# Kernel optimization log

Hardware: AMD Instinct MI355X
Metric: run time of the kernel (lower is better)

The kernel has to match this reference:

```python
import jax, jax.numpy as jnp
import numpy as np

N, E, D, H, A = 50000, 800000, 128, 256, 16


def setup_inputs() -> dict:
    key = jax.random.key(0)
    ks = jax.random.split(key, 16)
    s = 0.05
    return {
        "x": jax.random.normal(ks[0], (N, D), jnp.float32),
        "edge_index": jax.random.randint(ks[1], (2, E), 0, N, dtype=jnp.int32),
        "edge_attr": jax.random.normal(ks[2], (E, A), jnp.float32),
        # GCNConv 1 (input_dim -> hidden_dim): lin weight (no bias) + conv bias
        "W1": jax.random.normal(ks[3], (D, H), jnp.float32) * s,
        "b1": jnp.zeros((H,), jnp.float32),
        # GCNConv 2 (hidden_dim -> input_dim)
        "W2": jax.random.normal(ks[4], (H, D), jnp.float32) * s,
        "b2": jnp.zeros((D,), jnp.float32),
        # output_layer MLP: D -> H -> D
        "Wo1": jax.random.normal(ks[5], (D, H), jnp.float32) * s,
        "bo1": jnp.zeros((H,), jnp.float32),
        "Wo2": jax.random.normal(ks[6], (H, D), jnp.float32) * s,
        "bo2": jnp.zeros((D,), jnp.float32),
        # edge_predictor MLP: 2D+A -> H -> A
        "We1": jax.random.normal(ks[7], (2 * D + A, H), jnp.float32) * s,
        "be1": jnp.zeros((H,), jnp.float32),
        "We2": jax.random.normal(ks[8], (H, A), jnp.float32) * s,
        "be2": jnp.zeros((A,), jnp.float32),
    }


def reference(x, edge_index, edge_attr, W1, b1, W2, b2, Wo1, bo1, Wo2, bo2,
              We1, be1, We2, be2):
    n = x.shape[0]
    row, col = edge_index[0], edge_index[1]
    # GCNConv default: add self-loops, symmetric normalization deg^-1/2 A deg^-1/2
    loop = jnp.arange(n, dtype=row.dtype)
    row_f = jnp.concatenate([row, loop])
    col_f = jnp.concatenate([col, loop])
    deg = jax.ops.segment_sum(jnp.ones_like(col_f, dtype=x.dtype), col_f,
                              num_segments=n)
    dinv = jnp.where(deg > 0, jax.lax.rsqrt(jnp.maximum(deg, 1.0)), 0.0)
    norm = dinv[row_f] * dinv[col_f]  # [E+N]

    def gcn(h, W, b):
        h = h @ W                                # [n, out]
        msg = h[row_f] * norm[:, None]           # gather + scale
        agg = jax.ops.segment_sum(msg, col_f, num_segments=n)  # scatter-add
        return agg + b

    h = jax.nn.relu(gcn(x, W1, b1))
    h = jax.nn.relu(gcn(h, W2, b2))
    h = jax.nn.relu(h @ Wo1 + bo1) @ Wo2 + bo2   # output_layer MLP

    # edge predictor: gather endpoint features, concat with edge_attr, MLP
    edge_input = jnp.concatenate([h[row], h[col], edge_attr], axis=1)
    ea = jax.nn.relu(edge_input @ We1 + be1) @ We2 + be2
    return h, ea
```

## Files before the change

kernel.cpp:

```cpp
#include <hip/hip_runtime.h>
#include <hip/hip_bf16.h>

#define N_NODES 50000
#define N_EDGES 800000
#define DIM_D   128
#define DIM_H   256
#define DIM_A   16

typedef unsigned short u16;
typedef __attribute__((ext_vector_type(4))) float f4;
typedef __attribute__((ext_vector_type(8))) short s8;
typedef __attribute__((ext_vector_type(4))) short s4;

__device__ __forceinline__ u16 f2bf(float f) {
    union { float f; unsigned u; } v; v.f = f;
    unsigned r = v.u + 0x7FFFu + ((v.u >> 16) & 1u);
    return (u16)(r >> 16);
}
__device__ __forceinline__ float bf2f(u16 s) {
    union { unsigned u; float f; } v; v.u = ((unsigned)s) << 16; return v.f;
}
__device__ __forceinline__ s8 zero_s8() {
    s8 v;
#pragma unroll
    for (int i = 0; i < 8; i++) v[i] = 0;
    return v;
}
__device__ __forceinline__ s4 pk_bf16x4(float a, float b, float c, float d) {
    __hip_bfloat162 h0 = __float22bfloat162_rn(make_float2(a, b));
    __hip_bfloat162 h1 = __float22bfloat162_rn(make_float2(c, d));
    s4 v;
    __builtin_memcpy(&v, &h0, 4);
    __builtin_memcpy(((char*)&v) + 4, &h1, 4);
    return v;
}
__device__ __forceinline__ u16 f2bf_hw(float f) {
    __hip_bfloat16 h = __float2bfloat16(f);
    u16 u; __builtin_memcpy(&u, &h, 2);
    return u;
}

__device__ __forceinline__ int pq_off(int mt, int q) {
    return (mt >> 2) * 64 + ((mt >> 1) & 1) * 32 + q * 8 + (mt & 1) * 4;
}

__global__ __launch_bounds__(256) void k_zero(int* __restrict__ cnt) {
    int i = blockIdx.x * 256 + threadIdx.x;
    if (i < N_NODES) cnt[i] = 0;
}
__global__ __launch_bounds__(256) void k_count(const int* __restrict__ coli, int* __restrict__ cnt) {
    int e = blockIdx.x * 256 + threadIdx.x;
    if (e < N_EDGES) atomicAdd(&cnt[coli[e]], 1);
}
__global__ __launch_bounds__(256) void k_dinv(const int* __restrict__ cnt, float* __restrict__ dinv) {
    int i = blockIdx.x * 256 + threadIdx.x;
    if (i < N_NODES) dinv[i] = rsqrtf((float)(cnt[i] + 1));
}

#define SCAN_C 49
__global__ __launch_bounds__(1024) void k_scan(const int* __restrict__ cnt, int* __restrict__ start) {
    __shared__ int ps[1024];
    int t = threadIdx.x;
    int base = t * SCAN_C;
    int sum = 0;
    for (int i = 0; i < SCAN_C; i++) {
        int idx = base + i;
        sum += (idx < N_NODES) ? cnt[idx] : 0;
    }
    ps[t] = sum;
    __syncthreads();
    for (int ofs = 1; ofs < 1024; ofs <<= 1) {
        int v = (t >= ofs) ? ps[t - ofs] : 0;
        __syncthreads();
        ps[t] += v;
        __syncthreads();
    }
    int run = (t > 0) ? ps[t - 1] : 0;
    for (int i = 0; i < SCAN_C; i++) {
        int idx = base + i;
        if (idx < N_NODES) {
            start[idx] = run;
            run += cnt[idx];
        }
    }
    if (t == 1023) start[N_NODES] = ps[1023];
}
__global__ __launch_bounds__(256) void k_copy(const int* __restrict__ start, int* __restrict__ cursor) {
    int i = blockIdx.x * 256 + threadIdx.x;
    if (i < N_NODES) cursor[i] = start[i];
}
__global__ __launch_bounds__(256) void k_fill(const int* __restrict__ rowi, const int* __restrict__ coli,
                                              const float* __restrict__ dinv,
                                              int* __restrict__ cursor, int2* __restrict__ pack,
                                              int2* __restrict__ eidx) {
    int e = blockIdx.x * 256 + threadIdx.x;
    if (e >= N_EDGES) return;
    int r = rowi[e], c = coli[e];
    int slot = atomicAdd(&cursor[c], 1);
    float w = dinv[r] * dinv[c];
    pack[slot] = make_int2(r, __float_as_int(w));
    eidx[slot] = make_int2(e, c);
}

__global__ __launch_bounds__(256) void k_cast(const float* __restrict__ X, u16* __restrict__ Y, int n4) {
    int i = blockIdx.x * 256 + threadIdx.x;
    if (i >= n4) return;
    float4 v = *(const float4*)&X[(size_t)i * 4];
    ushort4 o;
    o.x = f2bf(v.x); o.y = f2bf(v.y); o.z = f2bf(v.z); o.w = f2bf(v.w);
    *(ushort4*)&Y[(size_t)i * 4] = o;
}

template <bool OB>
__global__ __launch_bounds__(256) void k_gather(const u16* __restrict__ X,
                                                const int2* __restrict__ pack,
                                                const int* __restrict__ start,
                                                const float* __restrict__ dinv,
                                                void* __restrict__ zout) {
    int node = blockIdx.x * 4 + (threadIdx.x >> 6);
    if (node >= N_NODES) return;
    int lane = threadIdx.x & 63;
    int half = lane >> 5, j = lane & 31;
    int c4 = j * 4;
    float di = dinv[node];
    f4 acc = {0.f, 0.f, 0.f, 0.f};
    if (half == 0) {
        float sl = di * di;
        ushort4 u = *(const ushort4*)&X[(size_t)node * DIM_D + c4];
        acc[0] = bf2f(u.x) * sl; acc[1] = bf2f(u.y) * sl;
        acc[2] = bf2f(u.z) * sl; acc[3] = bf2f(u.w) * sl;
    }
    int s0 = start[node], e0 = start[node + 1];
    int h0 = (e0 - s0 + 1) >> 1;
    int i   = half ? (s0 + h0) : s0;
    int end = half ? e0 : (s0 + h0);
    for (; i + 3 < end; i += 4) {
        int2 p0 = pack[i], p1 = pack[i + 1], p2 = pack[i + 2], p3 = pack[i + 3];
        ushort4 u0 = *(const ushort4*)&X[(size_t)p0.x * DIM_D + c4];
        ushort4 u1 = *(const ushort4*)&X[(size_t)p1.x * DIM_D + c4];
        ushort4 u2 = *(const ushort4*)&X[(size_t)p2.x * DIM_D + c4];
        ushort4 u3 = *(const ushort4*)&X[(size_t)p3.x * DIM_D + c4];
        float w0 = __int_as_float(p0.y), w1 = __int_as_float(p1.y);
        float w2 = __int_as_float(p2.y), w3 = __int_as_float(p3.y);
        acc[0] += bf2f(u0.x) * w0; acc[1] += bf2f(u0.y) * w0;
        acc[2] += bf2f(u0.z) * w0; acc[3] += bf2f(u0.w) * w0;
        acc[0] += bf2f(u1.x) * w1; acc[1] += bf2f(u1.y) * w1;
        acc[2] += bf2f(u1.z) * w1; acc[3] += bf2f(u1.w) * w1;
        acc[0] += bf2f(u2.x) * w2; acc[1] += bf2f(u2.y) * w2;
        acc[2] += bf2f(u2.z) * w2; acc[3] += bf2f(u2.w) * w2;
        acc[0] += bf2f(u3.x) * w3; acc[1] += bf2f(u3.y) * w3;
        acc[2] += bf2f(u3.z) * w3; acc[3] += bf2f(u3.w) * w3;
    }
    for (; i < end; i++) {
        int2 p = pack[i];
        float w = __int_as_float(p.y);
        ushort4 u = *(const ushort4*)&X[(size_t)p.x * DIM_D + c4];
        acc[0] += bf2f(u.x) * w; acc[1] += bf2f(u.y) * w;
        acc[2] += bf2f(u.z) * w; acc[3] += bf2f(u.w) * w;
    }
    float t0 = acc[0] + __shfl(acc[0], j + 32);
    float t1 = acc[1] + __shfl(acc[1], j + 32);
    float t2 = acc[2] + __shfl(acc[2], j + 32);
    float t3 = acc[3] + __shfl(acc[3], j + 32);
    if (half == 0) {
        if (OB) {
            s4 o = pk_bf16x4(t0, t1, t2, t3);
            *(s4*)&((u16*)zout)[(size_t)node * DIM_D + c4] = o;
        } else {
            *(float4*)&((float*)zout)[(size_t)node * DIM_D + c4] = make_float4(t0, t1, t2, t3);
        }
    }
}

__global__ __launch_bounds__(256) void k_twt(const float* __restrict__ W, u16* __restrict__ Wt,
                                             int K, int Nn) {
    int idx = blockIdx.x * 256 + threadIdx.x;
    if (idx >= K * Nn) return;
    int k = idx / Nn, n = idx - k * Nn;
    Wt[n * K + k] = f2bf(W[idx]);
}

__global__ __launch_bounds__(256) void k_bpq(const float* __restrict__ be1, float* __restrict__ bpq) {
    int i = blockIdx.x * 256 + threadIdx.x;
    if (i < 512) bpq[i] = (i < 256) ? be1[i] : 0.f;
}

#define BM 128
#define BK 32
#define BKP 56

template <int BNv, bool A_BF16, bool PRE_BR, bool POST_RELU, bool OUT_BF16, bool PERM_PQ>
__global__ __launch_bounds__(256) void k_gemm(const void* __restrict__ Ap,
                                              const u16* __restrict__ Wt,
                                              const float* __restrict__ preB,
                                              const float* __restrict__ postB,
                                              void* __restrict__ Cp,
                                              int M, int K, int Nn) {
    constexpr int BNT = BNv / 16;
    __shared__ __align__(16) u16 As[BM * BKP];
    __shared__ __align__(16) u16 Bs[BNv * BKP];
    const int tid = threadIdx.x;
    const int wid = tid >> 6, lane = tid & 63;
    const int q = lane >> 4, l = lane & 15;
    const int bm = blockIdx.x * BM, bn = blockIdx.y * BNv;

    f4 acc[2 * BNT];
#pragma unroll
    for (int i = 0; i < 2 * BNT; i++) { f4 zz = {0.f, 0.f, 0.f, 0.f}; acc[i] = zz; }

    for (int k0 = 0; k0 < K; k0 += BK) {
        __syncthreads();
#pragma unroll
        for (int p = 0; p < BNv / 64; p++) {
            int n = (tid >> 2) + p * 64, kc = (tid & 3) * 8;
            *(int4*)&Bs[n * BKP + kc] = *(const int4*)&Wt[(size_t)(bn + n) * K + k0 + kc];
        }
        if (A_BF16) {
            const u16* A = (const u16*)Ap;
#pragma unroll
            for (int p = 0; p < 2; p++) {
                int m = (tid >> 2) + p * 64, kc = (tid & 3) * 8;
                int gm = bm + m; if (gm >= M) gm = M - 1;
                *(int4*)&As[m * BKP + kc] = *(const int4*)&A[(size_t)gm * K + k0 + kc];
            }
        } else {
            const float* A = (const float*)Ap;
#pragma unroll
            for (int p = 0; p < 4; p++) {
                int m = (tid >> 3) + p * 32, k4 = (tid & 7) * 4;
                int gm = bm + m; if (gm >= M) gm = M - 1;
                float4 v = *(const float4*)&A[(size_t)gm * K + k0 + k4];
                if (PRE_BR) {
                    const float4 pb = *(const float4*)&preB[k0 + k4];
                    v.x = fmaxf(v.x + pb.x, 0.f);
                    v.y = fmaxf(v.y + pb.y, 0.f);
                    v.z = fmaxf(v.z + pb.z, 0.f);
                    v.w = fmaxf(v.w + pb.w, 0.f);
                }
                s4 o = pk_bf16x4(v.x, v.y, v.z, v.w);
                *(s4*)&As[m * BKP + k4] = o;
            }
        }
        __syncthreads();

        s8 af[2], bf[BNT];
#pragma unroll
        for (int mt = 0; mt < 2; mt++)
            af[mt] = *(const s8*)&As[(wid * 32 + mt * 16 + l) * BKP + q * 8];
#pragma unroll
        for (int nt = 0; nt < BNT; nt++)
            bf[nt] = *(const s8*)&Bs[(nt * 16 + l) * BKP + q * 8];
#pragma unroll
        for (int mt = 0; mt < 2; mt++)
#pragma unroll
            for (int nt = 0; nt < BNT; nt++)
                acc[mt * BNT + nt] = __builtin_amdgcn_mfma_f32_16x16x32_bf16(
                    af[mt], bf[nt], acc[mt * BNT + nt], 0, 0, 0);
    }

#pragma unroll
    for (int mt = 0; mt < 2; mt++) {
#pragma unroll
        for (int nt = 0; nt < BNT; nt++) {
            int colg = bn + nt * 16 + l;
            float pb = postB ? postB[colg] : 0.0f;
            int cols = colg;
            if (PERM_PQ) {
                int w = colg & 63, mtL = w >> 4;
                cols = (colg & ~63) | (((mtL >> 1) & 1) * 32) | (((w >> 2) & 3) * 8)
                       | ((mtL & 1) * 4) | (w & 3);
            }
#pragma unroll
            for (int r = 0; r < 4; r++) {
                int rowg = bm + wid * 32 + mt * 16 + q * 4 + r;
                if (rowg < M) {
                    float v = acc[mt * BNT + nt][r] + pb;
                    if (POST_RELU) v = fmaxf(v, 0.f);
                    if (OUT_BF16)
                        ((u16*)Cp)[(size_t)rowg * Nn + cols] = f2bf_hw(v);
                    else
                        ((float*)Cp)[(size_t)rowg * Nn + cols] = v;
                }
            }
        }
    }
}

#if __has_builtin(__builtin_amdgcn_mfma_f32_16x16x16bf16_1k)
#define KEEP4(a,b,c,d) asm volatile("" :: "v"(a), "v"(b), "v"(c), "v"(d))
__global__ __launch_bounds__(256) void k_edge(const u16* __restrict__ PQ,
                                              const float* __restrict__ attr,
                                              const int2* __restrict__ pack,
                                              const int2* __restrict__ eidx,
                                              const u16* __restrict__ Wct,
                                              const u16* __restrict__ We2t,
                                              const float* __restrict__ be2,
                                              float* __restrict__ outp) {
    __shared__ __align__(16) u16 lw[16 * 64 * 8];
    const int tid = threadIdx.x, wid = tid >> 6, lane = tid & 63;
    const int q = lane >> 4, l = lane & 15;
    for (int u = tid; u < 1024; u += 256) {
        int smt = u >> 6, sq = (u >> 4) & 3, sl = u & 15;
        *(uint2*)&lw[u * 8]     = *(const uint2*)&Wct[(smt * 16 + sl) * 16 + sq * 4];
        *(uint2*)&lw[u * 8 + 4] = *(const uint2*)&We2t[sl * DIM_H + smt * 16 + sq * 4];
    }
    __syncthreads();

    const float4 be2v = *(const float4*)&be2[q * 4];
    const int NT = N_EDGES / 16;
    const int step = gridDim.x * 4;
    const int lbase = lane * 8;

    int tile = blockIdx.x * 4 + wid;
    if (tile >= NT) return;
    int2 pk = pack[tile * 16 + l];
    int2 ec = eidx[tile * 16 + l];

    for (; tile < NT; tile += step) {
        const int re = pk.x, e = ec.x, ce = ec.y;
        const u16* prow = PQ + (size_t)re * 512 + q * 8;
        const u16* qrow = PQ + (size_t)ce * 512 + 256 + q * 8;

        float4 av = *(const float4*)&attr[(size_t)e * DIM_A + q * 4];
        s8 pw[8], qw[8];
#pragma unroll
        for (int w = 0; w < 8; w++) {
            pw[w] = *(const s8*)(prow + w * 32);
            qw[w] = *(const s8*)(qrow + w * 32);
        }
        int ntile = tile + step;
        int ns = (ntile < NT) ? ntile * 16 + l : l;
        int2 pk_n = pack[ns];
        int2 ec_n = eidx[ns];
        KEEP4(pw[0], pw[1], pw[2], pw[3]);
        KEEP4(pw[4], pw[5], pw[6], pw[7]);
        KEEP4(qw[0], qw[1], qw[2], qw[3]);
        KEEP4(qw[4], qw[5], qw[6], qw[7]);
        __builtin_amdgcn_sched_barrier(0);

        s4 af = pk_bf16x4(av.x, av.y, av.z, av.w);

        f4 acc2 = {0.f, 0.f, 0.f, 0.f};
#pragma unroll
        for (int w = 0; w < 8; w++) {
#pragma unroll
            for (int s = 0; s < 2; s++) {
                const int mt = w * 2 + s;
                s8 wf = *(const s8*)&lw[mt * 512 + lbase];
                s4 wcf = {wf[0], wf[1], wf[2], wf[3]};
                s4 wef = {wf[4], wf[5], wf[6], wf[7]};
                f4 pqs;
                pqs[0] = bf2f((u16)pw[w][s * 4 + 0]) + bf2f((u16)qw[w][s * 4 + 0]);
                pqs[1] = bf2f((u16)pw[w][s * 4 + 1]) + bf2f((u16)qw[w][s * 4 + 1]);
                pqs[2] = bf2f((u16)pw[w][s * 4 + 2]) + bf2f((u16)qw[w][s * 4 + 2]);
                pqs[3] = bf2f((u16)pw[w][s * 4 + 3]) + bf2f((u16)qw[w][s * 4 + 3]);
                f4 acc = __builtin_amdgcn_mfma_f32_16x16x16bf16_1k(wcf, af, pqs, 0, 0, 0);
                s4 uf = pk_bf16x4(fmaxf(acc[0], 0.f), fmaxf(acc[1], 0.f),
                                  fmaxf(acc[2], 0.f), fmaxf(acc[3], 0.f));
                acc2 = __builtin_amdgcn_mfma_f32_16x16x16bf16_1k(wef, uf, acc2, 0, 0, 0);
            }
        }
        *(float4*)&outp[(size_t)e * DIM_A + q * 4] =
            make_float4(acc2[0] + be2v.x, acc2[1] + be2v.y,
                        acc2[2] + be2v.z, acc2[3] + be2v.w);
        pk = pk_n; ec = ec_n;
    }
}
#else
#define UPAD 268
__global__ __launch_bounds__(256) void k_edge(const u16* __restrict__ PQ,
                                              const float* __restrict__ attr,
                                              const int2* __restrict__ pack,
                                              const int2* __restrict__ eidx,
                                              const u16* __restrict__ Wct,
                                              const u16* __restrict__ We2t,
                                              const float* __restrict__ be2,
                                              float* __restrict__ outp) {
    __shared__ __align__(16) u16 ub[4][16][UPAD];
    const int tid = threadIdx.x, wid = tid >> 6, lane = tid & 63;
    const int q = lane >> 4, l = lane & 15;
    const float4 be2v = *(const float4*)&be2[q * 4];
    u16(*u)[UPAD] = ub[wid];

    s8 wcf[16];
#pragma unroll
    for (int mt = 0; mt < 16; mt++) {
        wcf[mt] = zero_s8();
        if (q < 2) wcf[mt] = *(const s8*)&Wct[(mt * 16 + l) * 16 + q * 8];
    }

    for (int tile = blockIdx.x * 4 + wid; tile < N_EDGES / 16; tile += gridDim.x * 4) {
        const int s = tile * 16 + l;
        const int2 pk = pack[s];
        const int2 ec = eidx[s];
        const int re = pk.x, e = ec.x, ce = ec.y;
        const u16* prow = PQ + (size_t)re * 512;
        const u16* qrow = PQ + (size_t)ce * 512 + 256;

        s8 af = zero_s8();
        if (q < 2) {
            const float* ap = &attr[(size_t)e * DIM_A + q * 8];
            float4 a0 = *(const float4*)ap;
            float4 a1 = *(const float4*)(ap + 4);
            af[0] = (short)f2bf(a0.x); af[1] = (short)f2bf(a0.y);
            af[2] = (short)f2bf(a0.z); af[3] = (short)f2bf(a0.w);
            af[4] = (short)f2bf(a1.x); af[5] = (short)f2bf(a1.y);
            af[6] = (short)f2bf(a1.z); af[7] = (short)f2bf(a1.w);
        }

#pragma unroll
        for (int mt = 0; mt < 16; mt++) {
            f4 cz = {0.f, 0.f, 0.f, 0.f};
            f4 acc = __builtin_amdgcn_mfma_f32_16x16x32_bf16(wcf[mt], af, cz, 0, 0, 0);
            ushort4 pu = *(const ushort4*)(prow + pq_off(mt, q));
            ushort4 qu = *(const ushort4*)(qrow + pq_off(mt, q));
            float t0 = bf2f(pu.x) + bf2f(qu.x) + acc[0];
            float t1 = bf2f(pu.y) + bf2f(qu.y) + acc[1];
            float t2 = bf2f(pu.z) + bf2f(qu.z) + acc[2];
            float t3 = bf2f(pu.w) + bf2f(qu.w) + acc[3];
            ushort4 o;
            o.x = f2bf(fmaxf(t0, 0.f)); o.y = f2bf(fmaxf(t1, 0.f));
            o.z = f2bf(fmaxf(t2, 0.f)); o.w = f2bf(fmaxf(t3, 0.f));
            *(ushort4*)&u[l][mt * 16 + q * 4] = o;
        }

        f4 acc2 = {0.f, 0.f, 0.f, 0.f};
#pragma unroll
        for (int ks = 0; ks < 8; ks++) {
            s8 uf = *(const s8*)&u[l][ks * 32 + q * 8];
            s8 wf = *(const s8*)&We2t[(size_t)l * DIM_H + ks * 32 + q * 8];
            acc2 = __builtin_amdgcn_mfma_f32_16x16x32_bf16(wf, uf, acc2, 0, 0, 0);
        }
        *(float4*)&outp[(size_t)e * DIM_A + q * 4] =
            make_float4(acc2[0] + be2v.x, acc2[1] + be2v.y,
                        acc2[2] + be2v.z, acc2[3] + be2v.w);
    }
}
#endif

extern "C" void kernel_launch(void* const* d_in, const int* in_sizes, int n_in,
                              void* d_out, int out_size, void* d_ws, size_t ws_size,
                              hipStream_t stream) {
    (void)in_sizes; (void)n_in; (void)out_size; (void)ws_size;
    const float* x    = (const float*)d_in[0];
    const int*   ei   = (const int*)d_in[1];
    const float* attr = (const float*)d_in[2];
    const float* W1   = (const float*)d_in[3];
    const float* b1   = (const float*)d_in[4];
    const float* W2   = (const float*)d_in[5];
    const float* b2   = (const float*)d_in[6];
    const float* Wo1  = (const float*)d_in[7];
    const float* bo1  = (const float*)d_in[8];
    const float* Wo2  = (const float*)d_in[9];
    const float* bo2  = (const float*)d_in[10];
    const float* We1  = (const float*)d_in[11];
    const float* be1  = (const float*)d_in[12];
    const float* We2  = (const float*)d_in[13];
    const float* be2  = (const float*)d_in[14];
    const int* rowi = ei;
    const int* coli = ei + N_EDGES;

    float* hout = (float*)d_out;
    float* eout = hout + (size_t)N_NODES * DIM_D;

    char* ws = (char*)d_ws;
    size_t off = 0;
    auto nxt = [&](size_t b) -> void* {
        void* p = ws + off; off = (off + b + 255) & ~(size_t)255; return p;
    };
    float* dinv = (float*)nxt((size_t)N_NODES * 4);
    int* cnt    = (int*)nxt((size_t)N_NODES * 4);
    int* startp = (int*)nxt((size_t)(N_NODES + 1) * 4);
    int* cursor = (int*)nxt((size_t)N_NODES * 4);
    int2* pack  = (int2*)nxt((size_t)N_EDGES * 8);
    int2* eidx  = (int2*)nxt((size_t)N_EDGES * 8);
    u16* W1t   = (u16*)nxt(128 * 256 * 2);
    u16* W2t   = (u16*)nxt(128 * 256 * 2);
    u16* Wo1t  = (u16*)nxt(128 * 256 * 2);
    u16* Wo2t  = (u16*)nxt(128 * 256 * 2);
    u16* Wabt  = (u16*)nxt(512 * 128 * 2);
    u16* Wct   = (u16*)nxt(256 * 16 * 2);
    u16* We2t  = (u16*)nxt(16 * 256 * 2);
    float* bpq = (float*)nxt(512 * 4);
    u16* xb    = (u16*)nxt((size_t)N_NODES * DIM_D * 2);
    float* z   = (float*)nxt((size_t)N_NODES * DIM_D * 4);
    u16* h1    = (u16*)nxt((size_t)N_NODES * DIM_H * 2);
    u16* yb    = (u16*)nxt((size_t)N_NODES * DIM_D * 2);
    u16* PQb = (u16*)z;
    u16* zb  = (u16*)z;

    const int gN = (N_NODES + 255) / 256;
    const int gE = (N_EDGES + 255) / 256;

    k_twt<<<(128 * 256 + 255) / 256, 256, 0, stream>>>(W1, W1t, 128, 256);
    k_twt<<<(128 * 256 + 255) / 256, 256, 0, stream>>>(W2, W2t, 256, 128);
    k_twt<<<(128 * 256 + 255) / 256, 256, 0, stream>>>(Wo1, Wo1t, 128, 256);
    k_twt<<<(128 * 256 + 255) / 256, 256, 0, stream>>>(Wo2, Wo2t, 256, 128);
    k_twt<<<(128 * 256 + 255) / 256, 256, 0, stream>>>(We1, Wabt, 128, 256);
    k_twt<<<(128 * 256 + 255) / 256, 256, 0, stream>>>(We1 + 128 * 256, Wabt + 256 * 128, 128, 256);
    k_twt<<<(16 * 256 + 255) / 256, 256, 0, stream>>>(We1 + 256 * 256, Wct, 16, 256);
    k_twt<<<(16 * 256 + 255) / 256, 256, 0, stream>>>(We2, We2t, 256, 16);
    k_bpq<<<2, 256, 0, stream>>>(be1, bpq);

    k_zero<<<gN, 256, 0, stream>>>(cnt);
    k_count<<<gE, 256, 0, stream>>>(coli, cnt);
    k_dinv<<<gN, 256, 0, stream>>>(cnt, dinv);
    k_scan<<<1, 1024, 0, stream>>>(cnt, startp);
    k_copy<<<gN, 256, 0, stream>>>(startp, cursor);
    k_fill<<<gE, 256, 0, stream>>>(rowi, coli, dinv, cursor, pack, eidx);

    k_cast<<<(N_NODES * DIM_D / 4 + 255) / 256, 256, 0, stream>>>(x, xb, N_NODES * DIM_D / 4);

    const int gG = (N_NODES + 3) / 4;
    k_gather<true><<<gG, 256, 0, stream>>>(xb, pack, startp, dinv, zb);
    k_gemm<128, true, false, true, true, false><<<dim3(391, 2), 256, 0, stream>>>(zb, W1t, nullptr, b1, h1, N_NODES, 128, 256);
    k_gemm<64, true, false, false, true, false><<<dim3(391, 2), 256, 0, stream>>>(h1, W2t, nullptr, nullptr, yb, N_NODES, 256, 128);
    k_gather<false><<<gG, 256, 0, stream>>>(yb, pack, startp, dinv, z);
    k_gemm<128, false, true, true, true, false><<<dim3(391, 2), 256, 0, stream>>>(z, Wo1t, b2, bo1, h1, N_NODES, 128, 256);
    k_gemm<64, true, false, false, false, false><<<dim3(391, 2), 256, 0, stream>>>(h1, Wo2t, nullptr, bo2, hout, N_NODES, 256, 128);
    k_gemm<128, false, false, false, true, true><<<dim3(391, 4), 256, 0, stream>>>(hout, Wabt, nullptr, bpq, PQb, N_NODES, 128, 512);
    k_edge<<<2048, 256, 0, stream>>>(PQb, attr, pack, eidx, Wct, We2t, be2, eout);
}
```

Baseline: 661.2 us.

## Merge setup kernels, compute dinv inline, and use nontemporal loads for streams

Merges the eight weight-transpose launches, the bias-pack launch and the count zeroing into one k_init kernel. The dinv and cursor-copy kernels are removed: the scan writes cursor directly, and fill and gather recompute rsqrt from the degree counts. Streamed edge data (indices, pack, eidx, attr, output) now uses nontemporal loads and stores to avoid polluting cache. The goal is fewer launches and less small-kernel overhead, at the cost of some redundant rsqrt arithmetic.

```diff
diff --git a/kernel.cpp b/kernel.cpp
--- a/kernel.cpp
+++ b/kernel.cpp
@@ -11,6 +11,7 @@
 typedef __attribute__((ext_vector_type(4))) float f4;
 typedef __attribute__((ext_vector_type(8))) short s8;
 typedef __attribute__((ext_vector_type(4))) short s4;
+typedef __attribute__((ext_vector_type(2))) int i2;
 
 __device__ __forceinline__ u16 f2bf(float f) {
     union { float f; unsigned u; } v; v.f = f;
@@ -44,21 +45,56 @@
     return (mt >> 2) * 64 + ((mt >> 1) & 1) * 32 + q * 8 + (mt & 1) * 4;
 }
 
-__global__ __launch_bounds__(256) void k_zero(int* __restrict__ cnt) {
-    int i = blockIdx.x * 256 + threadIdx.x;
-    if (i < N_NODES) cnt[i] = 0;
-}
+__global__ __launch_bounds__(256) void k_init(const float* __restrict__ W1, const float* __restrict__ W2,
+                                              const float* __restrict__ Wo1, const float* __restrict__ Wo2,
+                                              const float* __restrict__ We1, const float* __restrict__ We2,
+                                              const float* __restrict__ be1,
+                                              u16* __restrict__ W1t, u16* __restrict__ W2t,
+                                              u16* __restrict__ Wo1t, u16* __restrict__ Wo2t,
+                                              u16* __restrict__ Wabt, u16* __restrict__ Wct,
+                                              u16* __restrict__ We2t, float* __restrict__ bpq,
+                                              int* __restrict__ cnt) {
+    int idx = blockIdx.x * 256 + threadIdx.x;
+    if (idx < 32768) {
+        int k = idx >> 8, n = idx & 255;
+        W1t[n * 128 + k] = f2bf(W1[idx]);
+    } else if (idx < 65536) {
+        int r = idx - 32768, k = r >> 7, n = r & 127;
+        W2t[n * 256 + k] = f2bf(W2[r]);
+    } else if (idx < 98304) {
+        int r = idx - 65536, k = r >> 8, n = r & 255;
+        Wo1t[n * 128 + k] = f2bf(Wo1[r]);
+    } else if (idx < 131072) {
+        int r = idx - 98304, k = r >> 7, n = r & 127;
+        Wo2t[n * 256 + k] = f2bf(Wo2[r]);
+    } else if (idx < 163840) {
+        int r = idx - 131072, k = r >> 8, n = r & 255;
+        Wabt[n * 128 + k] = f2bf(We1[r]);
+    } else if (idx < 196608) {
+        int r = idx - 163840, k = r >> 8, n = r & 255;
+        Wabt[32768 + n * 128 + k] = f2bf(We1[32768 + r]);
+    } else if (idx < 200704) {
+        int r = idx - 196608, k = r >> 8, n = r & 255;
+        Wct[n * 16 + k] = f2bf(We1[65536 + r]);
+    } else if (idx < 204800) {
+        int r = idx - 200704, k = r >> 4, n = r & 15;
+        We2t[n * 256 + k] = f2bf(We2[r]);
+    } else if (idx < 205312) {
+        int i = idx - 204800;
+        bpq[i] = (i < 256) ? be1[i] : 0.f;
+    } else if (idx < 205312 + N_NODES) {
+        cnt[idx - 205312] = 0;
+    }
+}
+
 __global__ __launch_bounds__(256) void k_count(const int* __restrict__ coli, int* __restrict__ cnt) {
     int e = blockIdx.x * 256 + threadIdx.x;
-    if (e < N_EDGES) atomicAdd(&cnt[coli[e]], 1);
-}
-__global__ __launch_bounds__(256) void k_dinv(const int* __restrict__ cnt, float* __restrict__ dinv) {
-    int i = blockIdx.x * 256 + threadIdx.x;
-    if (i < N_NODES) dinv[i] = rsqrtf((float)(cnt[i] + 1));
+    if (e < N_EDGES) atomicAdd(&cnt[__builtin_nontemporal_load(&coli[e])], 1);
 }
 
 #define SCAN_C 49
-__global__ __launch_bounds__(1024) void k_scan(const int* __restrict__ cnt, int* __restrict__ start) {
+__global__ __launch_bounds__(1024) void k_scan(const int* __restrict__ cnt, int* __restrict__ start,
+                                               int* __restrict__ cursor) {
     __shared__ int ps[1024];
     int t = threadIdx.x;
     int base = t * SCAN_C;
@@ -80,24 +116,23 @@
         int idx = base + i;
         if (idx < N_NODES) {
             start[idx] = run;
+            cursor[idx] = run;
             run += cnt[idx];
         }
     }
     if (t == 1023) start[N_NODES] = ps[1023];
 }
-__global__ __launch_bounds__(256) void k_copy(const int* __restrict__ start, int* __restrict__ cursor) {
-    int i = blockIdx.x * 256 + threadIdx.x;
-    if (i < N_NODES) cursor[i] = start[i];
-}
+
 __global__ __launch_bounds__(256) void k_fill(const int* __restrict__ rowi, const int* __restrict__ coli,
-                                              const float* __restrict__ dinv,
+                                              const int* __restrict__ cnt,
                                               int* __restrict__ cursor, int2* __restrict__ pack,
                                               int2* __restrict__ eidx) {
     int e = blockIdx.x * 256 + threadIdx.x;
     if (e >= N_EDGES) return;
-    int r = rowi[e], c = coli[e];
+    int r = __builtin_nontemporal_load(&rowi[e]);
+    int c = __builtin_nontemporal_load(&coli[e]);
     int slot = atomicAdd(&cursor[c], 1);
-    float w = dinv[r] * dinv[c];
+    float w = rsqrtf((float)(cnt[r] + 1)) * rsqrtf((float)(cnt[c] + 1));
     pack[slot] = make_int2(r, __float_as_int(w));
     eidx[slot] = make_int2(e, c);
 }
@@ -105,9 +140,9 @@
 __global__ __launch_bounds__(256) void k_cast(const float* __restrict__ X, u16* __restrict__ Y, int n4) {
     int i = blockIdx.x * 256 + threadIdx.x;
     if (i >= n4) return;
-    float4 v = *(const float4*)&X[(size_t)i * 4];
+    f4 v = __builtin_nontemporal_load((const f4*)&X[(size_t)i * 4]);
     ushort4 o;
-    o.x = f2bf(v.x); o.y = f2bf(v.y); o.z = f2bf(v.z); o.w = f2bf(v.w);
+    o.x = f2bf(v[0]); o.y = f2bf(v[1]); o.z = f2bf(v[2]); o.w = f2bf(v[3]);
     *(ushort4*)&Y[(size_t)i * 4] = o;
 }
 
@@ -115,14 +150,14 @@
 __global__ __launch_bounds__(256) void k_gather(const u16* __restrict__ X,
                                                 const int2* __restrict__ pack,
                                                 const int* __restrict__ start,
-                                                const float* __restrict__ dinv,
+                                                const int* __restrict__ cnt,
                                                 void* __restrict__ zout) {
     int node = blockIdx.x * 4 + (threadIdx.x >> 6);
     if (node >= N_NODES) return;
     int lane = threadIdx.x & 63;
     int half = lane >> 5, j = lane & 31;
     int c4 = j * 4;
-    float di = dinv[node];
+    float di = rsqrtf((float)(cnt[node] + 1));
     f4 acc = {0.f, 0.f, 0.f, 0.f};
     if (half == 0) {
         float sl = di * di;
@@ -135,13 +170,16 @@
     int i   = half ? (s0 + h0) : s0;
     int end = half ? e0 : (s0 + h0);
     for (; i + 3 < end; i += 4) {
-        int2 p0 = pack[i], p1 = pack[i + 1], p2 = pack[i + 2], p3 = pack[i + 3];
-        ushort4 u0 = *(const ushort4*)&X[(size_t)p0.x * DIM_D + c4];
-        ushort4 u1 = *(const ushort4*)&X[(size_t)p1.x * DIM_D + c4];
-        ushort4 u2 = *(const ushort4*)&X[(size_t)p2.x * DIM_D + c4];
-        ushort4 u3 = *(const ushort4*)&X[(size_t)p3.x * DIM_D + c4];
-        float w0 = __int_as_float(p0.y), w1 = __int_as_float(p1.y);
-        float w2 = __int_as_float(p2.y), w3 = __int_as_float(p3.y);
+        i2 p0 = __builtin_nontemporal_load((const i2*)&pack[i]);
+        i2 p1 = __builtin_nontemporal_load((const i2*)&pack[i + 1]);
+        i2 p2 = __builtin_nontemporal_load((const i2*)&pack[i + 2]);
+        i2 p3 = __builtin_nontemporal_load((const i2*)&pack[i + 3]);
+        ushort4 u0 = *(const ushort4*)&X[(size_t)p0[0] * DIM_D + c4];
+        ushort4 u1 = *(const ushort4*)&X[(size_t)p1[0] * DIM_D + c4];
+        ushort4 u2 = *(const ushort4*)&X[(size_t)p2[0] * DIM_D + c4];
+        ushort4 u3 = *(const ushort4*)&X[(size_t)p3[0] * DIM_D + c4];
+        float w0 = __int_as_float(p0[1]), w1 = __int_as_float(p1[1]);
+        float w2 = __int_as_float(p2[1]), w3 = __int_as_float(p3[1]);
         acc[0] += bf2f(u0.x) * w0; acc[1] += bf2f(u0.y) * w0;
         acc[2] += bf2f(u0.z) * w0; acc[3] += bf2f(u0.w) * w0;
         acc[0] += bf2f(u1.x) * w1; acc[1] += bf2f(u1.y) * w1;
@@ -152,9 +190,9 @@
         acc[2] += bf2f(u3.z) * w3; acc[3] += bf2f(u3.w) * w3;
     }
     for (; i < end; i++) {
-        int2 p = pack[i];
-        float w = __int_as_float(p.y);
-        ushort4 u = *(const ushort4*)&X[(size_t)p.x * DIM_D + c4];
+        i2 p = __builtin_nontemporal_load((const i2*)&pack[i]);
+        float w = __int_as_float(p[1]);
+        ushort4 u = *(const ushort4*)&X[(size_t)p[0] * DIM_D + c4];
         acc[0] += bf2f(u.x) * w; acc[1] += bf2f(u.y) * w;
         acc[2] += bf2f(u.z) * w; acc[3] += bf2f(u.w) * w;
     }
@@ -170,19 +208,6 @@
             *(float4*)&((float*)zout)[(size_t)node * DIM_D + c4] = make_float4(t0, t1, t2, t3);
         }
     }
-}
-
-__global__ __launch_bounds__(256) void k_twt(const float* __restrict__ W, u16* __restrict__ Wt,
-                                             int K, int Nn) {
-    int idx = blockIdx.x * 256 + threadIdx.x;
-    if (idx >= K * Nn) return;
-    int k = idx / Nn, n = idx - k * Nn;
-    Wt[n * K + k] = f2bf(W[idx]);
-}
-
-__global__ __launch_bounds__(256) void k_bpq(const float* __restrict__ be1, float* __restrict__ bpq) {
-    int i = blockIdx.x * 256 + threadIdx.x;
-    if (i < 512) bpq[i] = (i < 256) ? be1[i] : 0.f;
 }
 
 #define BM 128
@@ -313,15 +338,15 @@
 
     int tile = blockIdx.x * 4 + wid;
     if (tile >= NT) return;
-    int2 pk = pack[tile * 16 + l];
-    int2 ec = eidx[tile * 16 + l];
+    i2 pk = __builtin_nontemporal_load((const i2*)&pack[tile * 16 + l]);
+    i2 ec = __builtin_nontemporal_load((const i2*)&eidx[tile * 16 + l]);
 
     for (; tile < NT; tile += step) {
-        const int re = pk.x, e = ec.x, ce = ec.y;
+        const int re = pk[0], e = ec[0], ce = ec[1];
         const u16* prow = PQ + (size_t)re * 512 + q * 8;
         const u16* qrow = PQ + (size_t)ce * 512 + 256 + q * 8;
 
-        float4 av = *(const float4*)&attr[(size_t)e * DIM_A + q * 4];
+        f4 av = __builtin_nontemporal_load((const f4*)&attr[(size_t)e * DIM_A + q * 4]);
         s8 pw[8], qw[8];
 #pragma unroll
         for (int w = 0; w < 8; w++) {
@@ -330,15 +355,15 @@
         }
         int ntile = tile + step;
         int ns = (ntile < NT) ? ntile * 16 + l : l;
-        int2 pk_n = pack[ns];
-        int2 ec_n = eidx[ns];
+        i2 pk_n = __builtin_nontemporal_load((const i2*)&pack[ns]);
+        i2 ec_n = __builtin_nontemporal_load((const i2*)&eidx[ns]);
         KEEP4(pw[0], pw[1], pw[2], pw[3]);
         KEEP4(pw[4], pw[5], pw[6], pw[7]);
         KEEP4(qw[0], qw[1], qw[2], qw[3]);
         KEEP4(qw[4], qw[5], qw[6], qw[7]);
         __builtin_amdgcn_sched_barrier(0);
 
-        s4 af = pk_bf16x4(av.x, av.y, av.z, av.w);
+        s4 af = pk_bf16x4(av[0], av[1], av[2], av[3]);
 
         f4 acc2 = {0.f, 0.f, 0.f, 0.f};
 #pragma unroll
@@ -360,9 +385,8 @@
                 acc2 = __builtin_amdgcn_mfma_f32_16x16x16bf16_1k(wef, uf, acc2, 0, 0, 0);
             }
         }
-        *(float4*)&outp[(size_t)e * DIM_A + q * 4] =
-            make_float4(acc2[0] + be2v.x, acc2[1] + be2v.y,
-                        acc2[2] + be2v.z, acc2[3] + be2v.w);
+        f4 ov = {acc2[0] + be2v.x, acc2[1] + be2v.y, acc2[2] + be2v.z, acc2[3] + be2v.w};
+        __builtin_nontemporal_store(ov, (f4*)&outp[(size_t)e * DIM_A + q * 4]);
         pk = pk_n; ec = ec_n;
     }
 }
@@ -468,7 +492,6 @@
     auto nxt = [&](size_t b) -> void* {
         void* p = ws + off; off = (off + b + 255) & ~(size_t)255; return p;
     };
-    float* dinv = (float*)nxt((size_t)N_NODES * 4);
     int* cnt    = (int*)nxt((size_t)N_NODES * 4);
     int* startp = (int*)nxt((size_t)(N_NODES + 1) * 4);
     int* cursor = (int*)nxt((size_t)N_NODES * 4);
@@ -489,33 +512,23 @@
     u16* PQb = (u16*)z;
     u16* zb  = (u16*)z;
 
-    const int gN = (N_NODES + 255) / 256;
     const int gE = (N_EDGES + 255) / 256;
 
-    k_twt<<<(128 * 256 + 255) / 256, 256, 0, stream>>>(W1, W1t, 128, 256);
-    k_twt<<<(128 * 256 + 255) / 256, 256, 0, stream>>>(W2, W2t, 256, 128);
-    k_twt<<<(128 * 256 + 255) / 256, 256, 0, stream>>>(Wo1, Wo1t, 128, 256);
-    k_twt<<<(128 * 256 + 255) / 256, 256, 0, stream>>>(Wo2, Wo2t, 256, 128);
-    k_twt<<<(128 * 256 + 255) / 256, 256, 0, stream>>>(We1, Wabt, 128, 256);
-    k_twt<<<(128 * 256 + 255) / 256, 256, 0, stream>>>(We1 + 128 * 256, Wabt + 256 * 128, 128, 256);
-    k_twt<<<(16 * 256 + 255) / 256, 256, 0, stream>>>(We1 + 256 * 256, Wct, 16, 256);
-    k_twt<<<(16 * 256 + 255) / 256, 256, 0, stream>>>(We2, We2t, 256, 16);
-    k_bpq<<<2, 256, 0, stream>>>(be1, bpq);
-
-    k_zero<<<gN, 256, 0, stream>>>(cnt);
+    k_init<<<(205312 + N_NODES + 255) / 256, 256, 0, stream>>>(
+        W1, W2, Wo1, Wo2, We1, We2, be1,
+        W1t, W2t, Wo1t, Wo2t, Wabt, Wct, We2t, bpq, cnt);
+
     k_count<<<gE, 256, 0, stream>>>(coli, cnt);
-    k_dinv<<<gN, 256, 0, stream>>>(cnt, dinv);
-    k_scan<<<1, 1024, 0, stream>>>(cnt, startp);
-    k_copy<<<gN, 256, 0, stream>>>(startp, cursor);
-    k_fill<<<gE, 256, 0, stream>>>(rowi, coli, dinv, cursor, pack, eidx);
+    k_scan<<<1, 1024, 0, stream>>>(cnt, startp, cursor);
+    k_fill<<<gE, 256, 0, stream>>>(rowi, coli, cnt, cursor, pack, eidx);
 
     k_cast<<<(N_NODES * DIM_D / 4 + 255) / 256, 256, 0, stream>>>(x, xb, N_NODES * DIM_D / 4);
 
     const int gG = (N_NODES + 3) / 4;
-    k_gather<true><<<gG, 256, 0, stream>>>(xb, pack, startp, dinv, zb);
+    k_gather<true><<<gG, 256, 0, stream>>>(xb, pack, startp, cnt, zb);
     k_gemm<128, true, false, true, true, false><<<dim3(391, 2), 256, 0, stream>>>(zb, W1t, nullptr, b1, h1, N_NODES, 128, 256);
     k_gemm<64, true, false, false, true, false><<<dim3(391, 2), 256, 0, stream>>>(h1, W2t, nullptr, nullptr, yb, N_NODES, 256, 128);
-    k_gather<false><<<gG, 256, 0, stream>>>(yb, pack, startp, dinv, z);
+    k_gather<false><<<gG, 256, 0, stream>>>(yb, pack, startp, cnt, z);
     k_gemm<128, false, true, true, true, false><<<dim3(391, 2), 256, 0, stream>>>(z, Wo1t, b2, bo1, h1, N_NODES, 128, 256);
     k_gemm<64, true, false, false, false, false><<<dim3(391, 2), 256, 0, stream>>>(h1, Wo2t, nullptr, bo2, hout, N_NODES, 256, 128);
     k_gemm<128, false, false, false, true, true><<<dim3(391, 4), 256, 0, stream>>>(hout, Wabt, nullptr, bpq, PQb, N_NODES, 128, 512);
```

Measured after the change: 678.9 us. 2.7% more time.
